# Optimization experiments

Hardware: AMD Instinct MI355X
Metric: run time of the kernel (lower is better)

The kernel has to match this reference:

```python
import jax, jax.numpy as jnp
import numpy as np

B, T, C = 4, 4096, 1024
H = 16            # num_heads from init_kwargs
D = C // H        # head_dim = 64
W_SCALE = 0.02    # realistic init scale for weights


def setup_inputs() -> dict:
    key = jax.random.key(0)
    ks = jax.random.split(key, 9)
    inp = {"x": jax.random.normal(ks[0], (B, T, C), dtype=jnp.float32)}
    for i, nm in enumerate(["q", "k", "v", "o"]):
        inp[f"W{nm}"] = jax.random.normal(ks[1 + i], (C, C), dtype=jnp.float32) * W_SCALE
        inp[f"b{nm}"] = jnp.zeros((C,), dtype=jnp.float32)
    return inp


def reference(x, Wq, bq, Wk, bk, Wv, bv, Wo, bo):
    Bx, Tx, Cx = x.shape
    # projections (torch Linear: y = x @ W.T + b), split heads
    q = (x @ Wq.T + bq).reshape(Bx, Tx, H, D)
    k = (x @ Wk.T + bk).reshape(Bx, Tx, H, D)
    v = (x @ Wv.T + bv).reshape(Bx, Tx, H, D)
    # ELU+1 feature map
    q = jax.nn.elu(q) + 1.0
    k = jax.nn.elu(k) + 1.0
    # global KV aggregation: kv[b,h,d,e] = sum_t k[b,t,h,d] * v[b,t,h,e]
    kv = jnp.einsum('bthd,bthe->bhde', k, v)
    # normalizer: q . (sum_t k)
    denom = jnp.einsum('bthd,bhd->bth', q, k.sum(axis=1))
    num = jnp.einsum('bthd,bhde->bthe', q, kv)
    out = num / jnp.clip(denom, 1e-6, None)[..., None]
    out = out.reshape(Bx, Tx, Cx)
    return out @ Wo.T + bo
```

## Files before the change

### kernel.cpp

```cpp
#include <hip/hip_runtime.h>
#include <hip/hip_bf16.h>
#include <stdint.h>


#define B_ 4
#define T_ 4096
#define C_ 1024
#define H_ 16
#define D_ 64
#define M_ (B_*T_)
#define TCH 512
#define K_ 1024
#define NT_ (K_/64)

using u16 = unsigned short;
using u32 = unsigned int;

typedef __attribute__((ext_vector_type(8))) short bf16x8;
typedef __attribute__((ext_vector_type(4))) float f32x4;

static __device__ __forceinline__ u16 f2bf(float f){
  u32 u = __float_as_uint(f);
  u32 r = (u + 0x7fffu + ((u >> 16) & 1u)) >> 16;
  return (u16)r;
}
static __device__ __forceinline__ void unpack8(uint4 u, float* f){
  f[0]=__uint_as_float(u.x<<16); f[1]=__uint_as_float(u.x&0xffff0000u);
  f[2]=__uint_as_float(u.y<<16); f[3]=__uint_as_float(u.y&0xffff0000u);
  f[4]=__uint_as_float(u.z<<16); f[5]=__uint_as_float(u.z&0xffff0000u);
  f[6]=__uint_as_float(u.w<<16); f[7]=__uint_as_float(u.w&0xffff0000u);
}
static __device__ __forceinline__ void gload16(const u16* g, u16* l){
  __builtin_amdgcn_global_load_lds(
      (const __attribute__((address_space(1))) void*)g,
      (__attribute__((address_space(3))) void*)l, 16, 0, 0);
}

#define FENCE() asm volatile("" ::: "memory")
#define BAR() do { FENCE(); __builtin_amdgcn_s_barrier(); FENCE(); } while(0)

__global__ __launch_bounds__(256) void cvt_all(
    const float* __restrict__ x,
    const float* __restrict__ s0, const float* __restrict__ s1,
    const float* __restrict__ s2, const float* __restrict__ s3,
    u16* __restrict__ xb,
    u16* __restrict__ d0, u16* __restrict__ d1,
    u16* __restrict__ d2, u16* __restrict__ d3)
{
  const float* s; u16* d; int bi;
  if (blockIdx.x < 8192) { s = x; d = xb; bi = blockIdx.x; }
  else {
    const int seg = (blockIdx.x - 8192) >> 9;
    bi = (blockIdx.x - 8192) & 511;
    s = seg==0?s0:seg==1?s1:seg==2?s2:s3;
    d = seg==0?d0:seg==1?d1:seg==2?d2:d3;
  }
  const int i = (bi*256 + threadIdx.x) * 8;
  const float4 a = *(const float4*)(s + i);
  const float4 b = *(const float4*)(s + i + 4);
  uint4 o;
  o.x = (u32)f2bf(a.x) | ((u32)f2bf(a.y) << 16);
  o.y = (u32)f2bf(a.z) | ((u32)f2bf(a.w) << 16);
  o.z = (u32)f2bf(b.x) | ((u32)f2bf(b.y) << 16);
  o.w = (u32)f2bf(b.z) | ((u32)f2bf(b.w) << 16);
  *(uint4*)(d + i) = o;
}

template<bool FUSED>
__global__ __launch_bounds__(512, 2) void gemm256(
    const u16* __restrict__ X, const u16* __restrict__ Wm,
    const float* __restrict__ b0, const float* __restrict__ b1,
    const float* __restrict__ b2,
    void* __restrict__ Y0, void* __restrict__ Y1, void* __restrict__ Y2)
{
  extern __shared__ __align__(16) u16 lds[];
  const int tid  = threadIdx.x;
  const int lane = tid & 63, w = tid >> 6;
  const int wr = w >> 2, wc = w & 3;
  const int fr = lane & 15, hi = lane >> 4;

  const int xcd = blockIdx.x & 7;
  const int r   = blockIdx.x >> 3;
  const int ppx = gridDim.x >> 7;
  const int patchIdx = xcd * ppx + (r >> 4);
  const int wi = r & 15;
  const int pm = FUSED ? (patchIdx & 15) : patchIdx;
  const int pn = FUSED ? (patchIdx >> 4) : 0;
  const int bm = pm*4 + (wi & 3);
  const int bn = pn*4 + (wi >> 2);

  const int srow = tid >> 3;
  const int scc  = (tid & 7) ^ (srow & 7);
  const u16* gA = X  + (size_t)(bm*256 + srow)*K_ + scc*8;
  const u16* gB = Wm + (size_t)(bn*256 + srow)*K_ + scc*8;

  auto stageA = [&](int slot, int h, int kt){
    const u16* src = gA + (size_t)(h*128)*K_ + kt*64;
    u16* dst = lds + slot*16384 + h*8192 + tid*8;
    gload16(src, dst);
    gload16(src + (size_t)64*K_, dst + 4096);
  };
  auto stageB = [&](int slot, int h, int kt){
    const u16* src = gB + (size_t)(h*128)*K_ + kt*64;
    u16* dst = lds + 49152 + slot*16384 + h*8192 + tid*8;
    gload16(src, dst);
    gload16(src + (size_t)64*K_, dst + 4096);
  };

  f32x4 acc[8][4] = {};
  const int cx0 = (hi ^ (fr & 7)) << 3;
  const int cx1 = ((4 + hi) ^ (fr & 7)) << 3;
  const int br  = (wc & 1) * 64;

  stageA(0,0,0); stageA(0,1,0);
  stageB(0,0,0); stageB(0,1,0);
  stageA(1,0,1); stageA(1,1,1);
  stageB(1,0,1); stageB(1,1,1);
  asm volatile("s_waitcnt vmcnt(8)" ::: "memory");
  BAR();

  int aslot = 0;
  #pragma unroll 2
  for (int v = 0; v < NT_; ++v) {
    const int bslot  = v & 1;
    const int astage = (aslot == 0) ? 2 : aslot - 1;
    const bool more  = (v + 2 < NT_);
    const u16* As = lds + aslot*16384 + wr*8192;
    const u16* Bs = lds + 49152 + bslot*16384 + (wc>>1)*8192;

    bf16x8 a[4], bv0[4], bv1[4];

    #pragma unroll
    for (int j = 0; j < 4; ++j) bv0[j] = *(const bf16x8*)&Bs[(br + j*16 + fr)*64 + cx0];
    #pragma unroll
    for (int i = 0; i < 4; ++i) a[i]   = *(const bf16x8*)&As[(i*16 + fr)*64 + cx0];
    if (more) stageA(astage, 0, v+2);
    BAR();
    __builtin_amdgcn_s_setprio(1);
    #pragma unroll
    for (int i = 0; i < 4; ++i)
      #pragma unroll
      for (int j = 0; j < 4; ++j)
        acc[i][j] = __builtin_amdgcn_mfma_f32_16x16x32_bf16(a[i], bv0[j], acc[i][j], 0, 0, 0);
    __builtin_amdgcn_s_setprio(0);
    BAR();

    #pragma unroll
    for (int i = 0; i < 4; ++i) a[i] = *(const bf16x8*)&As[((4+i)*16 + fr)*64 + cx0];
    if (more) stageA(astage, 1, v+2);
    BAR();
    __builtin_amdgcn_s_setprio(1);
    #pragma unroll
    for (int i = 0; i < 4; ++i)
      #pragma unroll
      for (int j = 0; j < 4; ++j)
        acc[4+i][j] = __builtin_amdgcn_mfma_f32_16x16x32_bf16(a[i], bv0[j], acc[4+i][j], 0, 0, 0);
    __builtin_amdgcn_s_setprio(0);
    BAR();

    #pragma unroll
    for (int j = 0; j < 4; ++j) bv1[j] = *(const bf16x8*)&Bs[(br + j*16 + fr)*64 + cx1];
    #pragma unroll
    for (int i = 0; i < 4; ++i) a[i]   = *(const bf16x8*)&As[(i*16 + fr)*64 + cx1];
    if (more) stageB(bslot, 0, v+2);
    BAR();
    __builtin_amdgcn_s_setprio(1);
    #pragma unroll
    for (int i = 0; i < 4; ++i)
      #pragma unroll
      for (int j = 0; j < 4; ++j)
        acc[i][j] = __builtin_amdgcn_mfma_f32_16x16x32_bf16(a[i], bv1[j], acc[i][j], 0, 0, 0);
    __builtin_amdgcn_s_setprio(0);
    BAR();

    #pragma unroll
    for (int i = 0; i < 4; ++i) a[i] = *(const bf16x8*)&As[((4+i)*16 + fr)*64 + cx1];
    if (more) stageB(bslot, 1, v+2);
    BAR();
    __builtin_amdgcn_s_setprio(1);
    #pragma unroll
    for (int i = 0; i < 4; ++i)
      #pragma unroll
      for (int j = 0; j < 4; ++j)
        acc[4+i][j] = __builtin_amdgcn_mfma_f32_16x16x32_bf16(a[i], bv1[j], acc[4+i][j], 0, 0, 0);
    __builtin_amdgcn_s_setprio(0);
    if (v + 1 < NT_) {
      if (more) asm volatile("s_waitcnt vmcnt(8)" ::: "memory");
      else      asm volatile("s_waitcnt vmcnt(0)" ::: "memory");
      BAR();
    }
    aslot = (aslot == 2) ? 0 : aslot + 1;
  }

  const int nloc = wc*64 + fr;
  if constexpr (FUSED) {
    const int sel  = bn >> 2;
    const int colb = (bn & 3)*256 + nloc;
    const float* bp = (sel == 0 ? b0 : sel == 1 ? b1 : b2);
    u16* Y = (u16*)(sel == 0 ? Y0 : sel == 1 ? Y1 : Y2);
    const bool elu = sel < 2;
    float bb[4];
    #pragma unroll
    for (int j = 0; j < 4; ++j) bb[j] = bp[colb + j*16];
    #pragma unroll
    for (int i = 0; i < 8; ++i) {
      #pragma unroll
      for (int r2 = 0; r2 < 4; ++r2) {
        const size_t row = (size_t)(bm*256 + wr*128 + i*16 + hi*4 + r2);
        u16* yp = Y + row*1024 + colb;
        #pragma unroll
        for (int j = 0; j < 4; ++j) {
          float vv = acc[i][j][r2] + bb[j];
          if (elu) vv = (vv > 0.0f) ? (vv + 1.0f) : __expf(vv);
          yp[j*16] = f2bf(vv);
        }
      }
    }
  } else {
    const int n0 = bn*256 + nloc;
    float bb[4];
    #pragma unroll
    for (int j = 0; j < 4; ++j) bb[j] = b0[n0 + j*16];
    float* Y = (float*)Y0;
    #pragma unroll
    for (int i = 0; i < 8; ++i) {
      #pragma unroll
      for (int r2 = 0; r2 < 4; ++r2) {
        const size_t row = (size_t)(bm*256 + wr*128 + i*16 + hi*4 + r2);
        float* yp = Y + row*1024 + n0;
        #pragma unroll
        for (int j = 0; j < 4; ++j)
          yp[j*16] = acc[i][j][r2] + bb[j];
      }
    }
  }
}

__global__ __launch_bounds__(256) void kv_partial(
    const u16* __restrict__ Kb, const u16* __restrict__ Vb,
    float* __restrict__ kvp, float* __restrict__ ksp)
{
  const int tid = threadIdx.x;
  const int bh = blockIdx.x;
  const int b = bh >> 4, h = bh & 15;
  const int chunk = blockIdx.y;
  __shared__ float kbuf[32][68];
  __shared__ float vbuf[32][68];
  float acc[4][4] = {};
  float ksl = 0.0f;
  const int d0 = (tid >> 4) << 2, e0 = (tid & 15) << 2;
  const int lrow = tid >> 3, lcol = (tid & 7) << 3;

  for (int s = 0; s < TCH/32; ++s) {
    const int t = chunk*TCH + s*32;
    {
      const size_t base = ((size_t)(b*T_ + t + lrow))*C_ + h*64 + lcol;
      const uint4 ku = *(const uint4*)(Kb + base);
      const uint4 vu = *(const uint4*)(Vb + base);
      float kf[8], vf[8];
      unpack8(ku, kf); unpack8(vu, vf);
      #pragma unroll
      for (int j = 0; j < 8; ++j) { kbuf[lrow][lcol+j] = kf[j]; vbuf[lrow][lcol+j] = vf[j]; }
    }
    __syncthreads();
    if (tid < 64) {
      #pragma unroll
      for (int tt = 0; tt < 32; ++tt) ksl += kbuf[tt][tid];
    }
    #pragma unroll
    for (int tt = 0; tt < 32; ++tt) {
      const float4 ka = *(const float4*)&kbuf[tt][d0];
      const float4 va = *(const float4*)&vbuf[tt][e0];
      const float kr[4] = {ka.x, ka.y, ka.z, ka.w};
      const float vr[4] = {va.x, va.y, va.z, va.w};
      #pragma unroll
      for (int i = 0; i < 4; ++i)
        #pragma unroll
        for (int j = 0; j < 4; ++j)
          acc[i][j] = fmaf(kr[i], vr[j], acc[i][j]);
    }
    __syncthreads();
  }

  float* dst = kvp + ((size_t)(chunk*64 + bh))*4096;
  #pragma unroll
  for (int i = 0; i < 4; ++i)
    *(float4*)&dst[(d0+i)*64 + e0] = make_float4(acc[i][0], acc[i][1], acc[i][2], acc[i][3]);
  if (tid < 64) ksp[((size_t)(chunk*64 + bh))*64 + tid] = ksl;
}

__global__ __launch_bounds__(256) void kv_reduce(
    const float* __restrict__ kvp, const float* __restrict__ ksp,
    u16* __restrict__ kvT)
{
  const int idx = blockIdx.x*256 + threadIdx.x;
  if (idx < 262144) {
    float s = 0.0f;
    #pragma unroll
    for (int c = 0; c < 8; ++c) s += kvp[(size_t)c*262144 + idx];
    const int bh = idx >> 12, d = (idx >> 6) & 63, e = idx & 63;
    kvT[(size_t)bh*5120 + e*64 + d] = f2bf(s);
  } else if (idx < 266240) {
    const int i2 = idx - 262144;
    float s = 0.0f;
    #pragma unroll
    for (int c = 0; c < 8; ++c) s += ksp[(size_t)c*4096 + i2];
    const int bh = i2 >> 6, d = i2 & 63;
    kvT[(size_t)bh*5120 + 4096 + d] = f2bf(s);
  } else if (idx < 266240 + 64*15*64) {
    const int i3 = idx - 266240;
    const int bh = i3 / 960, rd = i3 - bh*960;
    kvT[(size_t)bh*5120 + 4160 + rd] = 0;
  }
}

__global__ __launch_bounds__(256) void attn_norm_mfma(
    const u16* __restrict__ Qb, const u16* __restrict__ kvT,
    u16* __restrict__ attn)
{
  __shared__ __align__(16) u16 qs[256*64];
  const int tid = threadIdx.x;
  const int lane = tid & 63, w = tid >> 6;
  const int bh = blockIdx.x;
  const int b = bh >> 4, h = bh & 15;
  const int tt = blockIdx.y;
  const int fr = lane & 15, hi = lane >> 4;

  {
    const int srow = tid >> 3, scc = tid & 7;
    #pragma unroll
    for (int r = 0; r < 8; ++r) {
      const int row = r*32 + srow;
      const u16* src = Qb + ((size_t)(b*T_ + tt*256 + row))*C_ + h*64
                         + ((scc ^ (row & 7)) << 3);
      gload16(src, qs + tid*8 + r*2048);
    }
  }

  const u16* kvb = kvT + (size_t)bh*5120;
  bf16x8 bv[5][2];
  #pragma unroll
  for (int j = 0; j < 5; ++j) {
    const int row = (j < 4) ? (j*16 + fr) : (64 + fr);
    bv[j][0] = *(const bf16x8*)&kvb[row*64 + hi*8];
    bv[j][1] = *(const bf16x8*)&kvb[row*64 + 32 + hi*8];
  }

  __syncthreads();

  f32x4 accN[4][4] = {};
  f32x4 accD[4] = {};
  #pragma unroll
  for (int kh = 0; kh < 2; ++kh) {
    const int cx = ((kh*4 + hi) ^ (fr & 7)) << 3;
    bf16x8 a[4];
    #pragma unroll
    for (int i = 0; i < 4; ++i)
      a[i] = *(const bf16x8*)&qs[(w*64 + i*16 + fr)*64 + cx];
    #pragma unroll
    for (int i = 0; i < 4; ++i) {
      #pragma unroll
      for (int j = 0; j < 4; ++j)
        accN[i][j] = __builtin_amdgcn_mfma_f32_16x16x32_bf16(a[i], bv[j][kh], accN[i][j], 0, 0, 0);
      accD[i] = __builtin_amdgcn_mfma_f32_16x16x32_bf16(a[i], bv[4][kh], accD[i], 0, 0, 0);
    }
  }

  #pragma unroll
  for (int i = 0; i < 4; ++i) {
    #pragma unroll
    for (int r = 0; r < 4; ++r) {
      const float den = __shfl(accD[i][r], lane & 0x30);
      const float inv = 1.0f / fmaxf(den, 1e-6f);
      const size_t row = (size_t)(b*T_ + tt*256 + w*64 + i*16 + hi*4 + r);
      u16* yp = attn + row*1024 + h*64 + fr;
      #pragma unroll
      for (int j = 0; j < 4; ++j)
        yp[j*16] = f2bf(accN[i][j][r] * inv);
    }
  }
}

extern "C" void kernel_launch(void* const* d_in, const int* in_sizes, int n_in,
                              void* d_out, int out_size, void* d_ws, size_t ws_size,
                              hipStream_t stream)
{
  (void)in_sizes; (void)n_in; (void)out_size; (void)ws_size;
  const float* x  = (const float*)d_in[0];
  const float* Wq = (const float*)d_in[1];
  const float* bq = (const float*)d_in[2];
  const float* Wk = (const float*)d_in[3];
  const float* bk = (const float*)d_in[4];
  const float* Wv = (const float*)d_in[5];
  const float* bv = (const float*)d_in[6];
  const float* Wo = (const float*)d_in[7];
  const float* bo = (const float*)d_in[8];
  float* out = (float*)d_out;
  char* ws = (char*)d_ws;

  const size_t MB = 1024*1024;
  u16*   xb   = (u16*)(ws);
  u16*   wqb  = (u16*)(ws + 32*MB);
  u16*   wkb  = (u16*)(ws + 34*MB);
  u16*   wvb  = (u16*)(ws + 36*MB);
  u16*   wob  = (u16*)(ws + 38*MB);
  u16*   q    = (u16*)(ws + 40*MB);
  u16*   k    = (u16*)(ws + 72*MB);
  u16*   v    = (u16*)(ws + 104*MB);
  float* kvp  = (float*)(ws + 136*MB);
  float* ksp  = (float*)(ws + 144*MB);
  u16*   kvT  = (u16*)(ws + 144*MB + 131072);
  u16*   attn = xb;

  static bool s_attr_done = false;
  if (!s_attr_done) {
    (void)hipFuncSetAttribute(reinterpret_cast<const void*>(gemm256<true>),
                              hipFuncAttributeMaxDynamicSharedMemorySize, 163840);
    (void)hipFuncSetAttribute(reinterpret_cast<const void*>(gemm256<false>),
                              hipFuncAttributeMaxDynamicSharedMemorySize, 163840);
    s_attr_done = true;
  }

  dim3 blk(256);
  cvt_all<<<dim3(8192 + 4*512), blk, 0, stream>>>(
      x, Wq, Wk, Wv, Wo, xb, wqb, wkb, wvb, wob);

  gemm256<true><<<dim3(64*12), dim3(512), 163840, stream>>>(
      xb, wqb, bq, bk, bv, q, k, v);

  kv_partial<<<dim3(B_*H_, T_/TCH), blk, 0, stream>>>(k, v, kvp, ksp);
  kv_reduce<<<dim3(1280), blk, 0, stream>>>(kvp, ksp, kvT);
  attn_norm_mfma<<<dim3(B_*H_, T_/256), blk, 0, stream>>>(q, kvT, attn);

  gemm256<false><<<dim3(64*4), dim3(512), 163840, stream>>>(
      attn, wob, bo, bo, bo, out, out, out);
}
```

Before: 220.9 us.

## Use 16-wave 1024-thread GEMM blocks with 64x64 wave tiles and double buffering

Restructures the 256x256 bf16 GEMM to run 1024 threads (16 waves) per block, each wave owning a 64x64 output tile instead of 128x64. The A/B pipeline moves from triple-buffered A plus double-buffered B with staggered half-stage loads to a plain double buffer that loads full A and B K-slices at once, cutting LDS to 128KB. The aim is more waves in flight to hide memory and LDS latency. In exchange each wave reuses less data per LDS read, the loop now waits for all outstanding loads every iteration, and the register budget per thread is tighter.

```diff
diff --git a/kernel.cpp b/kernel.cpp
--- a/kernel.cpp
+++ b/kernel.cpp
@@ -67,7 +67,7 @@
 }
 
 template<bool FUSED>
-__global__ __launch_bounds__(512, 2) void gemm256(
+__global__ __launch_bounds__(1024, 4) void gemm256(
     const u16* __restrict__ X, const u16* __restrict__ Wm,
     const float* __restrict__ b0, const float* __restrict__ b1,
     const float* __restrict__ b2,
@@ -93,103 +93,69 @@
   const int scc  = (tid & 7) ^ (srow & 7);
   const u16* gA = X  + (size_t)(bm*256 + srow)*K_ + scc*8;
   const u16* gB = Wm + (size_t)(bn*256 + srow)*K_ + scc*8;
-
-  auto stageA = [&](int slot, int h, int kt){
-    const u16* src = gA + (size_t)(h*128)*K_ + kt*64;
-    u16* dst = lds + slot*16384 + h*8192 + tid*8;
-    gload16(src, dst);
-    gload16(src + (size_t)64*K_, dst + 4096);
+  u16* const ldst = lds + tid*8;
+
+  auto stage = [&](int slot, int kt){
+    const size_t ko = (size_t)kt * 64;
+    gload16(gA + ko,                 ldst + slot*16384);
+    gload16(gA + (size_t)128*K_ + ko, ldst + slot*16384 + 8192);
+    gload16(gB + ko,                 ldst + 32768 + slot*16384);
+    gload16(gB + (size_t)128*K_ + ko, ldst + 32768 + slot*16384 + 8192);
   };
-  auto stageB = [&](int slot, int h, int kt){
-    const u16* src = gB + (size_t)(h*128)*K_ + kt*64;
-    u16* dst = lds + 49152 + slot*16384 + h*8192 + tid*8;
-    gload16(src, dst);
-    gload16(src + (size_t)64*K_, dst + 4096);
-  };
-
-  f32x4 acc[8][4] = {};
+
+  const int ah = wr >> 1, arow0 = (wr & 1) * 64;
+  const int bh = wc >> 1, brow0 = (wc & 1) * 64;
   const int cx0 = (hi ^ (fr & 7)) << 3;
   const int cx1 = ((4 + hi) ^ (fr & 7)) << 3;
-  const int br  = (wc & 1) * 64;
-
-  stageA(0,0,0); stageA(0,1,0);
-  stageB(0,0,0); stageB(0,1,0);
-  stageA(1,0,1); stageA(1,1,1);
-  stageB(1,0,1); stageB(1,1,1);
-  asm volatile("s_waitcnt vmcnt(8)" ::: "memory");
+  const u16* pA[2][2], *pB[2][2];
+  #pragma unroll
+  for (int s = 0; s < 2; ++s) {
+    pA[s][0] = lds + s*16384 + ah*8192 + (arow0 + fr)*64 + cx0;
+    pA[s][1] = lds + s*16384 + ah*8192 + (arow0 + fr)*64 + cx1;
+    pB[s][0] = lds + 32768 + s*16384 + bh*8192 + (brow0 + fr)*64 + cx0;
+    pB[s][1] = lds + 32768 + s*16384 + bh*8192 + (brow0 + fr)*64 + cx1;
+  }
+
+  f32x4 acc[4][4] = {};
+
+  stage(0, 0);
+  asm volatile("s_waitcnt vmcnt(0)" ::: "memory");
   BAR();
 
-  int aslot = 0;
   #pragma unroll 2
   for (int v = 0; v < NT_; ++v) {
-    const int bslot  = v & 1;
-    const int astage = (aslot == 0) ? 2 : aslot - 1;
-    const bool more  = (v + 2 < NT_);
-    const u16* As = lds + aslot*16384 + wr*8192;
-    const u16* Bs = lds + 49152 + bslot*16384 + (wc>>1)*8192;
-
-    bf16x8 a[4], bv0[4], bv1[4];
-
-    #pragma unroll
-    for (int j = 0; j < 4; ++j) bv0[j] = *(const bf16x8*)&Bs[(br + j*16 + fr)*64 + cx0];
-    #pragma unroll
-    for (int i = 0; i < 4; ++i) a[i]   = *(const bf16x8*)&As[(i*16 + fr)*64 + cx0];
-    if (more) stageA(astage, 0, v+2);
+    const int s = v & 1;
+    bf16x8 a[4], b[4];
+
+    #pragma unroll
+    for (int i = 0; i < 4; ++i) a[i] = *(const bf16x8*)&pA[0][0][s*16384 + i*1024];
+    #pragma unroll
+    for (int j = 0; j < 4; ++j) b[j] = *(const bf16x8*)&pB[0][0][s*16384 + j*1024];
+    if (v + 1 < NT_) stage(s^1, v+1);
     BAR();
     __builtin_amdgcn_s_setprio(1);
     #pragma unroll
     for (int i = 0; i < 4; ++i)
       #pragma unroll
       for (int j = 0; j < 4; ++j)
-        acc[i][j] = __builtin_amdgcn_mfma_f32_16x16x32_bf16(a[i], bv0[j], acc[i][j], 0, 0, 0);
+        acc[i][j] = __builtin_amdgcn_mfma_f32_16x16x32_bf16(a[i], b[j], acc[i][j], 0, 0, 0);
     __builtin_amdgcn_s_setprio(0);
     BAR();
 
     #pragma unroll
-    for (int i = 0; i < 4; ++i) a[i] = *(const bf16x8*)&As[((4+i)*16 + fr)*64 + cx0];
-    if (more) stageA(astage, 1, v+2);
+    for (int i = 0; i < 4; ++i) a[i] = *(const bf16x8*)&pA[0][1][s*16384 + i*1024];
+    #pragma unroll
+    for (int j = 0; j < 4; ++j) b[j] = *(const bf16x8*)&pB[0][1][s*16384 + j*1024];
     BAR();
     __builtin_amdgcn_s_setprio(1);
     #pragma unroll
     for (int i = 0; i < 4; ++i)
       #pragma unroll
       for (int j = 0; j < 4; ++j)
-        acc[4+i][j] = __builtin_amdgcn_mfma_f32_16x16x32_bf16(a[i], bv0[j], acc[4+i][j], 0, 0, 0);
+        acc[i][j] = __builtin_amdgcn_mfma_f32_16x16x32_bf16(a[i], b[j], acc[i][j], 0, 0, 0);
     __builtin_amdgcn_s_setprio(0);
+    if (v + 1 < NT_) asm volatile("s_waitcnt vmcnt(0)" ::: "memory");
     BAR();
-
-    #pragma unroll
-    for (int j = 0; j < 4; ++j) bv1[j] = *(const bf16x8*)&Bs[(br + j*16 + fr)*64 + cx1];
-    #pragma unroll
-    for (int i = 0; i < 4; ++i) a[i]   = *(const bf16x8*)&As[(i*16 + fr)*64 + cx1];
-    if (more) stageB(bslot, 0, v+2);
-    BAR();
-    __builtin_amdgcn_s_setprio(1);
-    #pragma unroll
-    for (int i = 0; i < 4; ++i)
-      #pragma unroll
-      for (int j = 0; j < 4; ++j)
-        acc[i][j] = __builtin_amdgcn_mfma_f32_16x16x32_bf16(a[i], bv1[j], acc[i][j], 0, 0, 0);
-    __builtin_amdgcn_s_setprio(0);
-    BAR();
-
-    #pragma unroll
-    for (int i = 0; i < 4; ++i) a[i] = *(const bf16x8*)&As[((4+i)*16 + fr)*64 + cx1];
-    if (more) stageB(bslot, 1, v+2);
-    BAR();
-    __builtin_amdgcn_s_setprio(1);
-    #pragma unroll
-    for (int i = 0; i < 4; ++i)
-      #pragma unroll
-      for (int j = 0; j < 4; ++j)
-        acc[4+i][j] = __builtin_amdgcn_mfma_f32_16x16x32_bf16(a[i], bv1[j], acc[4+i][j], 0, 0, 0);
-    __builtin_amdgcn_s_setprio(0);
-    if (v + 1 < NT_) {
-      if (more) asm volatile("s_waitcnt vmcnt(8)" ::: "memory");
-      else      asm volatile("s_waitcnt vmcnt(0)" ::: "memory");
-      BAR();
-    }
-    aslot = (aslot == 2) ? 0 : aslot + 1;
   }
 
   const int nloc = wc*64 + fr;
@@ -203,10 +169,10 @@
     #pragma unroll
     for (int j = 0; j < 4; ++j) bb[j] = bp[colb + j*16];
     #pragma unroll
-    for (int i = 0; i < 8; ++i) {
+    for (int i = 0; i < 4; ++i) {
       #pragma unroll
       for (int r2 = 0; r2 < 4; ++r2) {
-        const size_t row = (size_t)(bm*256 + wr*128 + i*16 + hi*4 + r2);
+        const size_t row = (size_t)(bm*256 + wr*64 + i*16 + hi*4 + r2);
         u16* yp = Y + row*1024 + colb;
         #pragma unroll
         for (int j = 0; j < 4; ++j) {
@@ -223,10 +189,10 @@
     for (int j = 0; j < 4; ++j) bb[j] = b0[n0 + j*16];
     float* Y = (float*)Y0;
     #pragma unroll
-    for (int i = 0; i < 8; ++i) {
+    for (int i = 0; i < 4; ++i) {
       #pragma unroll
       for (int r2 = 0; r2 < 4; ++r2) {
-        const size_t row = (size_t)(bm*256 + wr*128 + i*16 + hi*4 + r2);
+        const size_t row = (size_t)(bm*256 + wr*64 + i*16 + hi*4 + r2);
         float* yp = Y + row*1024 + n0;
         #pragma unroll
         for (int j = 0; j < 4; ++j)
@@ -415,9 +381,9 @@
   static bool s_attr_done = false;
   if (!s_attr_done) {
     (void)hipFuncSetAttribute(reinterpret_cast<const void*>(gemm256<true>),
-                              hipFuncAttributeMaxDynamicSharedMemorySize, 163840);
+                              hipFuncAttributeMaxDynamicSharedMemorySize, 131072);
     (void)hipFuncSetAttribute(reinterpret_cast<const void*>(gemm256<false>),
-                              hipFuncAttributeMaxDynamicSharedMemorySize, 163840);
+                              hipFuncAttributeMaxDynamicSharedMemorySize, 131072);
     s_attr_done = true;
   }
 
@@ -425,13 +391,13 @@
   cvt_all<<<dim3(8192 + 4*512), blk, 0, stream>>>(
       x, Wq, Wk, Wv, Wo, xb, wqb, wkb, wvb, wob);
 
-  gemm256<true><<<dim3(64*12), dim3(512), 163840, stream>>>(
+  gemm256<true><<<dim3(64*12), dim3(1024), 131072, stream>>>(
       xb, wqb, bq, bk, bv, q, k, v);
 
   kv_partial<<<dim3(B_*H_, T_/TCH), blk, 0, stream>>>(k, v, kvp, ksp);
   kv_reduce<<<dim3(1280), blk, 0, stream>>>(kvp, ksp, kvT);
   attn_norm_mfma<<<dim3(B_*H_, T_/256), blk, 0, stream>>>(q, kvT, attn);
 
-  gemm256<false><<<dim3(64*4), dim3(512), 163840, stream>>>(
+  gemm256<false><<<dim3(64*4), dim3(1024), 131072, stream>>>(
       attn, wob, bo, bo, bo, out, out, out);
 }
```

After: 290.0 us. 31.3% more time.
